# Kernel optimization log

Measured on AMD Instinct MI355X. Metric: run time of the kernel, lower is better.

## Reference

```python
import jax, jax.numpy as jnp
import numpy as np

N = 1024
NODE_DIM = 3
HIDDEN = 128
NLAYERS = 3
HEADS = 4
HD = HIDDEN // HEADS  # 32
EPS = 1e-5
NEG = -1e9


def setup_inputs() -> dict:
    key = jax.random.key(0)
    ks = jax.random.split(key, 32)
    def w(k, shape, fan_in):
        return jax.random.normal(k, shape, jnp.float32) / np.sqrt(fan_in).astype(np.float32)
    node_features = jax.random.normal(ks[0], (N, NODE_DIM), jnp.float32)
    adj = jax.random.randint(ks[1], (N, N), 0, 2).astype(jnp.float32)
    adj = adj.at[jnp.arange(N), jnp.arange(N)].set(1.0)  # self-loops
    inp = dict(
        node_features=node_features,
        adj=adj,
        Wp=w(ks[2], (NODE_DIM, HIDDEN), NODE_DIM), bp=jnp.zeros((HIDDEN,), jnp.float32),
        Wl=w(ks[3], (NLAYERS, HIDDEN, HIDDEN), HIDDEN),
        Wr=w(ks[4], (NLAYERS, HIDDEN, HIDDEN), HIDDEN),
        Wv=w(ks[5], (NLAYERS, HIDDEN, HIDDEN), HIDDEN),
        att=w(ks[6], (NLAYERS, HD), HD),
        gamma=jnp.ones((NLAYERS, HIDDEN), jnp.float32),
        beta=jnp.zeros((NLAYERS, HIDDEN), jnp.float32),
        Wn1=w(ks[7], (HIDDEN, 64), HIDDEN), bn1=jnp.zeros((64,), jnp.float32),
        Wn2=w(ks[8], (64, 1), 64), bn2=jnp.zeros((1,), jnp.float32),
        Wd1=w(ks[9], (HIDDEN, 64), HIDDEN), bd1=jnp.zeros((64,), jnp.float32),
        Wd2=w(ks[10], (64, 2), 64), bd2=jnp.zeros((2,), jnp.float32),
        Wv1=w(ks[11], (HIDDEN, 64), HIDDEN), bv1=jnp.zeros((64,), jnp.float32),
        Wv2=w(ks[12], (64, 1), 64), bv2=jnp.zeros((1,), jnp.float32),
    )
    return inp


def _gat_layer(h, mask, Wl, Wr, Wv, att, gamma, beta):
    n = h.shape[0]
    wlh = (h @ Wl).reshape(n, HEADS, HD)
    wrh = (h @ Wr).reshape(n, HEADS, HD)
    # pair[i,j,h,d] = LeakyReLU(Wl h_i + Wr h_j)  -- the O(N^2 H D) tensor
    pair = jax.nn.leaky_relu(wlh[:, None, :, :] + wrh[None, :, :, :], 0.2)
    e = jnp.einsum('ijhd,d->ijh', pair, att)
    e = jnp.where(mask[:, :, None], e, NEG)
    alpha = jax.nn.softmax(e, axis=1)  # softmax over neighbours j (dropout = identity in eval)
    v = (h @ Wv).reshape(n, HEADS, HD)
    agg = jnp.einsum('ijh,jhd->ihd', alpha, v).reshape(n, HIDDEN)
    mu = agg.mean(-1, keepdims=True)
    var = agg.var(-1, keepdims=True)
    out = (agg - mu) / jnp.sqrt(var + EPS) * gamma + beta
    return jax.nn.relu(out)


def reference(node_features, adj, Wp, bp, Wl, Wr, Wv, att, gamma, beta,
              Wn1, bn1, Wn2, bn2, Wd1, bd1, Wd2, bd2, Wv1, bv1, Wv2, bv2):
    mask = adj > 0.5
    h = jax.nn.relu(node_features @ Wp + bp)
    for l in range(NLAYERS):
        h = h + _gat_layer(h, mask, Wl[l], Wr[l], Wv[l], att[l], gamma[l], beta[l])
    node_logits = (jax.nn.relu(h @ Wn1 + bn1) @ Wn2 + bn2).squeeze(-1)
    delta_mu = jax.nn.relu(h @ Wd1 + bd1) @ Wd2 + bd2
    pooled = h.mean(axis=0)
    value = (jax.nn.relu(pooled @ Wv1 + bv1) @ Wv2 + bv2).squeeze(-1)
    return (node_logits, delta_mu, value)
```

## Files before the change

kernel.cpp:

```cpp
#include <hip/hip_runtime.h>
#include <hip/hip_bf16.h>

#define NN 1024
#define HID 128
#define NHEADS 4
#define HDD 32
#define NL 3

constexpr int OFF_CONV = 16;
constexpr int OFF_NF   = OFF_CONV;
constexpr int OFF_WP   = OFF_NF  + 3072;
constexpr int OFF_BP   = OFF_WP  + 384;
constexpr int OFF_WL   = OFF_BP  + 128;
constexpr int OFF_WR   = OFF_WL  + 49152;
constexpr int OFF_WVW  = OFF_WR  + 49152;
constexpr int OFF_ATT  = OFF_WVW + 49152;
constexpr int OFF_GAM  = OFF_ATT + 96;
constexpr int OFF_BET  = OFF_GAM + 384;
constexpr int OFF_WN1  = OFF_BET + 384;
constexpr int OFF_BN1  = OFF_WN1 + 8192;
constexpr int OFF_WN2  = OFF_BN1 + 64;
constexpr int OFF_BN2  = OFF_WN2 + 64;
constexpr int OFF_WD1  = OFF_BN2 + 1;
constexpr int OFF_BD1  = OFF_WD1 + 8192;
constexpr int OFF_WD2  = OFF_BD1 + 64;
constexpr int OFF_BD2  = OFF_WD2 + 128;
constexpr int OFF_WV1  = OFF_BD2 + 2;
constexpr int OFF_BV1  = OFF_WV1 + 8192;
constexpr int OFF_WV2  = OFF_BV1 + 64;
constexpr int OFF_BV2  = OFF_WV2 + 64;
constexpr int OFF_CONV_END = OFF_BV2 + 1;
constexpr int CONV_TOTAL = OFF_CONV_END - OFF_CONV;
constexpr int CB = (CONV_TOTAL + 255) / 256;
constexpr int OFF_MASK = 176960;
constexpr int OFF_H    = OFF_MASK + NN*32;
constexpr int OFF_WLH  = OFF_H   + NN*HID;
constexpr int OFF_WRH  = OFF_WLH + NN*HID;
constexpr int OFF_WVH  = OFF_WRH + NN*HID;
constexpr int OFF_CL   = OFF_WVH + NN*HID;
constexpr int OFF_CR   = OFF_CL  + NHEADS*NN;

__device__ __forceinline__ float bf2f(unsigned short u) {
    return __uint_as_float(((unsigned)u) << 16);
}
__device__ __forceinline__ void store_out(void* out, int idx, float v, bool bf) {
    if (bf) {
        unsigned u = __float_as_uint(v);
        unsigned r = (u + 0x7FFFu + ((u >> 16) & 1u)) >> 16;
        ((unsigned short*)out)[idx] = (unsigned short)r;
    } else {
        ((float*)out)[idx] = v;
    }
}
__device__ __forceinline__ float ldraw(const void* p, int idx, bool bf) {
    return bf ? bf2f(((const unsigned short*)p)[idx]) : ((const float*)p)[idx];
}
__device__ __forceinline__ bool detect_bf(const unsigned* nf) {
    unsigned w = nf[threadIdx.x & 63];
    int e = (int)((w >> 23) & 0xFFu);
    unsigned long long b = __ballot(e >= 110 && e <= 140);
    return __popcll(b) < 32;
}

struct P21 { const void* p[21]; };
__device__ const int g_sizes[21] = {3072,384,128,49152,49152,49152,96,384,384,
                                    8192,64,64,1,8192,64,128,2,8192,64,64,1};
__device__ const int g_dsts[21] = {OFF_NF,OFF_WP,OFF_BP,OFF_WL,OFF_WR,OFF_WVW,OFF_ATT,
                                   OFF_GAM,OFF_BET,OFF_WN1,OFF_BN1,OFF_WN2,OFF_BN2,
                                   OFF_WD1,OFF_BD1,OFF_WD2,OFF_BD2,OFF_WV1,OFF_BV1,
                                   OFF_WV2,OFF_BV2};

__global__ __launch_bounds__(256) void k_pre(P21 in, const void* adj, const unsigned* nf, float* ws) {
    bool bf = detect_bf(nf);
    int b = blockIdx.x, t = threadIdx.x;
    if (b < CB) {
        int g = b * 256 + t;
        if (g >= CONV_TOTAL) return;
        int rem = g, s = 0;
        while (s < 21 && rem >= g_sizes[s]) { rem -= g_sizes[s]; s++; }
        if (s >= 21) return;
        ws[g_dsts[s] + rem] = ldraw(in.p[s], rem, bf);
    } else if (b < CB + NN) {
        int i = b - CB;
        unsigned* mask = (unsigned*)(ws + OFF_MASK);
        int lane = t & 63, wv = t >> 6;
        #pragma unroll
        for (int q = 0; q < 4; q++) {
            int seg = wv * 4 + q;
            int j = seg * 64 + lane;
            float v = ldraw(adj, i * NN + j, bf);
            unsigned long long bl = __ballot(v > 0.5f);
            if (lane == 0) {
                mask[i * 32 + seg * 2]     = (unsigned)bl;
                mask[i * 32 + seg * 2 + 1] = (unsigned)(bl >> 32);
            }
        }
    } else {
        int bb = b - CB - NN;
        int i = bb * 2 + (t >> 7), c = t & 127;
        float a = ldraw(in.p[2], c, bf);
        #pragma unroll
        for (int k = 0; k < 3; k++)
            a += ldraw(in.p[0], i * 3 + k, bf) * ldraw(in.p[1], k * HID + c, bf);
        ws[OFF_H + i * HID + c] = fmaxf(a, 0.0f);
    }
}

__global__ __launch_bounds__(128) void k_mm3(float* ws, int l) {
    __shared__ float hs[4][HID];
    int c = threadIdx.x, i0 = blockIdx.x * 4, which = blockIdx.y;
    const float* h = ws + OFF_H;
    #pragma unroll
    for (int r = 0; r < 4; r++) hs[r][c] = h[(i0 + r) * HID + c];
    __syncthreads();
    int woff = (which == 0) ? OFF_WL : (which == 1) ? OFF_WR : OFF_WVW;
    const float* W = ws + woff + l * HID * HID;
    float a[4] = {0,0,0,0};
    #pragma unroll 4
    for (int k = 0; k < HID; k++) {
        float w = W[k * HID + c];
        #pragma unroll
        for (int r = 0; r < 4; r++) a[r] += hs[r][k] * w;
    }
    if (which == 0) {
        #pragma unroll
        for (int r = 0; r < 4; r++) ws[OFF_WLH + (i0 + r) * HID + c] = a[r];
        float att = ws[OFF_ATT + l * HDD + (c & 31)];
        #pragma unroll
        for (int r = 0; r < 4; r++) {
            float t = att * a[r];
            #pragma unroll
            for (int off = 1; off < 32; off <<= 1) t += __shfl_xor(t, off, 64);
            if ((c & 31) == 0) ws[OFF_CL + (c >> 5) * NN + (i0 + r)] = 0.6f * t;
        }
    } else {
        int doff = (which == 1) ? OFF_WRH : OFF_WVH;
        #pragma unroll
        for (int r = 0; r < 4; r++)
            ws[doff + (c >> 2) * (NN * 4) + (i0 + r) * 4 + (c & 3)] = a[r];
        if (which == 1) {
            float att = ws[OFF_ATT + l * HDD + (c & 31)];
            #pragma unroll
            for (int r = 0; r < 4; r++) {
                float t = att * a[r];
                #pragma unroll
                for (int off = 1; off < 32; off <<= 1) t += __shfl_xor(t, off, 64);
                if ((c & 31) == 0) ws[OFF_CR + (c >> 5) * NN + (i0 + r)] = 0.6f * t;
            }
        }
    }
}

__global__ __launch_bounds__(512) void k_attn(float* ws, int l) {
    int t = threadIdx.x;
    int i0 = blockIdx.x * 4;
    int lane = t & 63;
    int w = t >> 6;
    int h = __builtin_amdgcn_readfirstlane(w & 3);
    int p = __builtin_amdgcn_readfirstlane(w >> 2);
    int iA = i0 + 2 * p, iB = iA + 1;

    __shared__ unsigned mrow[4][32];
    __shared__ float ebuf[8][64][33];
    __shared__ float invs[4][4];
    __shared__ float agg_s[4][HID];
    __shared__ float red2[4][2][2];

    if (t < 128) mrow[t >> 5][t & 31] = ((const unsigned*)(ws + OFF_MASK))[i0 * 32 + t];
    __syncthreads();

    unsigned mbA = 0, mbB = 0;
    #pragma unroll
    for (int jc = 0; jc < 16; jc++) {
        int wi = jc * 2 + (lane >> 5);
        mbA |= ((mrow[2 * p][wi] >> (lane & 31)) & 1u) << jc;
        mbB |= ((mrow[2 * p + 1][wi] >> (lane & 31)) & 1u) << jc;
    }

    float att_r[32], wlA[32], wlB[32];
    const float* attp = ws + OFF_ATT + l * HDD;
    const float* wlpA = ws + OFF_WLH + iA * HID + h * HDD;
    const float* wlpB = ws + OFF_WLH + iB * HID + h * HDD;
    #pragma unroll
    for (int d = 0; d < 32; d++) {
        att_r[d] = 0.4f * attp[d];
        wlA[d] = wlpA[d];
        wlB[d] = wlpB[d];
    }
    float clA = ws[OFF_CL + h * NN + iA];
    float clB = ws[OFF_CL + h * NN + iB];

    const float* wrT = ws + OFF_WRH + h * 8 * (NN * 4) + lane * 4;
    const float* wvT = ws + OFF_WVH + h * 8 * (NN * 4) + lane * 4;
    const float* crp = ws + OFF_CR + h * NN;

    float mA = -1e30f, mB = -1e30f;
    #pragma unroll 1
    for (int jc = 0; jc < 16; jc++) {
        float cr6 = crp[jc * 64 + lane];
        float dA = 0.0f, dB = 0.0f;
        #pragma unroll
        for (int dq = 0; dq < 8; dq++) {
            float4 wv4 = *(const float4*)(wrT + dq * (NN * 4) + jc * 256);
            dA = fmaf(att_r[dq*4+0], fabsf(wlA[dq*4+0] + wv4.x), dA);
            dB = fmaf(att_r[dq*4+0], fabsf(wlB[dq*4+0] + wv4.x), dB);
            dA = fmaf(att_r[dq*4+1], fabsf(wlA[dq*4+1] + wv4.y), dA);
            dB = fmaf(att_r[dq*4+1], fabsf(wlB[dq*4+1] + wv4.y), dB);
            dA = fmaf(att_r[dq*4+2], fabsf(wlA[dq*4+2] + wv4.z), dA);
            dB = fmaf(att_r[dq*4+2], fabsf(wlB[dq*4+2] + wv4.z), dB);
            dA = fmaf(att_r[dq*4+3], fabsf(wlA[dq*4+3] + wv4.w), dA);
            dB = fmaf(att_r[dq*4+3], fabsf(wlB[dq*4+3] + wv4.w), dB);
        }
        float eA = (clA + cr6) + dA; eA = ((mbA >> jc) & 1u) ? eA : -1e9f;
        float eB = (clB + cr6) + dB; eB = ((mbB >> jc) & 1u) ? eB : -1e9f;
        ebuf[w][lane][jc]      = eA;
        ebuf[w][lane][16 + jc] = eB;
        mA = fmaxf(mA, eA);
        mB = fmaxf(mB, eB);
    }
    #pragma unroll
    for (int off = 32; off > 0; off >>= 1) {
        mA = fmaxf(mA, __shfl_xor(mA, off, 64));
        mB = fmaxf(mB, __shfl_xor(mB, off, 64));
    }

    float accA[32], accB[32];
    #pragma unroll
    for (int d = 0; d < 32; d++) { accA[d] = 0.0f; accB[d] = 0.0f; }
    float lsA = 0.0f, lsB = 0.0f;
    #pragma unroll 1
    for (int jc = 0; jc < 16; jc++) {
        float peA = __expf(ebuf[w][lane][jc]      - mA);
        float peB = __expf(ebuf[w][lane][16 + jc] - mB);
        lsA += peA; lsB += peB;
        #pragma unroll
        for (int dq = 0; dq < 8; dq++) {
            float4 v4 = *(const float4*)(wvT + dq * (NN * 4) + jc * 256);
            accA[dq*4+0] = fmaf(peA, v4.x, accA[dq*4+0]);
            accB[dq*4+0] = fmaf(peB, v4.x, accB[dq*4+0]);
            accA[dq*4+1] = fmaf(peA, v4.y, accA[dq*4+1]);
            accB[dq*4+1] = fmaf(peB, v4.y, accB[dq*4+1]);
            accA[dq*4+2] = fmaf(peA, v4.z, accA[dq*4+2]);
            accB[dq*4+2] = fmaf(peB, v4.z, accB[dq*4+2]);
            accA[dq*4+3] = fmaf(peA, v4.w, accA[dq*4+3]);
            accB[dq*4+3] = fmaf(peB, v4.w, accB[dq*4+3]);
        }
    }
    #pragma unroll
    for (int off = 32; off > 0; off >>= 1) {
        lsA += __shfl_xor(lsA, off, 64);
        lsB += __shfl_xor(lsB, off, 64);
    }
    if (lane == 0) {
        invs[2 * p][h]     = 1.0f / lsA;
        invs[2 * p + 1][h] = 1.0f / lsB;
    }
    __syncthreads();

    float* rbuf = &ebuf[0][0][0];
    {
        int reg = p * 4 + h;
        #pragma unroll
        for (int d = 0; d < 32; d++) rbuf[(reg * 64 + lane) * 33 + d] = accA[d];
        __syncthreads();
        int g = t >> 6, d = lane & 31, half = lane >> 5;
        float s = 0.0f;
        #pragma unroll
        for (int lq = 0; lq < 32; lq++) s += rbuf[(g * 64 + half * 32 + lq) * 33 + d];
        s += __shfl_xor(s, 32, 64);
        int node = 2 * (g >> 2), hh = g & 3;
        if (half == 0) agg_s[node][hh * 32 + d] = s * invs[node][hh];
        __syncthreads();
    }
    {
        int reg = p * 4 + h;
        #pragma unroll
        for (int d = 0; d < 32; d++) rbuf[(reg * 64 + lane) * 33 + d] = accB[d];
        __syncthreads();
        int g = t >> 6, d = lane & 31, half = lane >> 5;
        float s = 0.0f;
        #pragma unroll
        for (int lq = 0; lq < 32; lq++) s += rbuf[(g * 64 + half * 32 + lq) * 33 + d];
        s += __shfl_xor(s, 32, 64);
        int node = 2 * (g >> 2) + 1, hh = g & 3;
        if (half == 0) agg_s[node][hh * 32 + d] = s * invs[node][hh];
        __syncthreads();
    }

    {
        int n = t >> 7, f = t & 127;
        float agg = agg_s[n][f];
        float s = agg, s2 = agg * agg;
        #pragma unroll
        for (int off = 32; off > 0; off >>= 1) {
            s  += __shfl_xor(s,  off, 64);
            s2 += __shfl_xor(s2, off, 64);
        }
        int half = (t >> 6) & 1;
        if (lane == 0) { red2[n][half][0] = s; red2[n][half][1] = s2; }
        __syncthreads();
        float ts  = red2[n][0][0] + red2[n][1][0];
        float ts2 = red2[n][0][1] + red2[n][1][1];
        float mu  = ts  * (1.0f / HID);
        float var = ts2 * (1.0f / HID) - mu * mu;
        float gm = ws[OFF_GAM + l * HID + f];
        float be = ws[OFF_BET + l * HID + f];
        float o = (agg - mu) * rsqrtf(var + 1e-5f) * gm + be;
        ws[OFF_H + (i0 + n) * HID + f] += fmaxf(o, 0.0f);
    }
}

__global__ __launch_bounds__(1024) void k_post(float* ws, const unsigned* nf, void* out) {
    bool bf = detect_bf(nf);
    int b = blockIdx.x, t = threadIdx.x;
    if (b < 64) {
        __shared__ float hrow[16][HID];
        int n = t >> 6, tt = t & 63;
        int i = b * 16 + n;
        hrow[n][tt]      = ws[OFF_H + i * HID + tt];
        hrow[n][tt + 64] = ws[OFF_H + i * HID + tt + 64];
        __syncthreads();
        const float* Wn1 = ws + OFF_WN1;
        const float* Wd1 = ws + OFF_WD1;
        float z1 = ws[OFF_BN1 + tt], zd = ws[OFF_BD1 + tt];
        #pragma unroll 4
        for (int k = 0; k < HID; k++) {
            float hk = hrow[n][k];
            z1 += hk * Wn1[k * 64 + tt];
            zd += hk * Wd1[k * 64 + tt];
        }
        z1 = fmaxf(z1, 0.0f); zd = fmaxf(zd, 0.0f);
        float lg = z1 * ws[OFF_WN2 + tt];
        float d0 = zd * ws[OFF_WD2 + tt * 2 + 0];
        float d1 = zd * ws[OFF_WD2 + tt * 2 + 1];
        #pragma unroll
        for (int off = 32; off > 0; off >>= 1) {
            lg += __shfl_xor(lg, off, 64);
            d0 += __shfl_xor(d0, off, 64);
            d1 += __shfl_xor(d1, off, 64);
        }
        if (tt == 0) {
            store_out(out, i,              lg + ws[OFF_BN2],     bf);
            store_out(out, NN + i * 2 + 0, d0 + ws[OFF_BD2 + 0], bf);
            store_out(out, NN + i * 2 + 1, d1 + ws[OFF_BD2 + 1], bf);
        }
    } else {
        __shared__ float part[8][HID];
        __shared__ float pooled[HID];
        int g = t >> 7, c = t & 127;
        float s = 0.0f;
        #pragma unroll 16
        for (int r = 0; r < 128; r++) s += ws[OFF_H + (g * 128 + r) * HID + c];
        part[g][c] = s;
        __syncthreads();
        if (t < HID) {
            float p = 0.0f;
            #pragma unroll
            for (int gg = 0; gg < 8; gg++) p += part[gg][t];
            pooled[t] = p * (1.0f / NN);
        }
        __syncthreads();
        if (t < 64) {
            float z = ws[OFF_BV1 + t];
            float z1 = 0.0f;
            #pragma unroll 8
            for (int k = 0; k < HID; k += 2) {
                z  += pooled[k]     * ws[OFF_WV1 + k * 64 + t];
                z1 += pooled[k + 1] * ws[OFF_WV1 + (k + 1) * 64 + t];
            }
            z = fmaxf(z + z1, 0.0f);
            float pv = z * ws[OFF_WV2 + t];
            #pragma unroll
            for (int off = 32; off > 0; off >>= 1) pv += __shfl_xor(pv, off, 64);
            if (t == 0) store_out(out, 3072, pv + ws[OFF_BV2], bf);
        }
    }
}

extern "C" void kernel_launch(void* const* d_in, const int* in_sizes, int n_in,
                              void* d_out, int out_size, void* d_ws, size_t ws_size,
                              hipStream_t stream) {
    float* ws = (float*)d_ws;
    const unsigned* nf = (const unsigned*)d_in[0];

    P21 ptrs;
    const int map[21] = {0,2,3,4,5,6,7,8,9,10,11,12,13,14,15,16,17,18,19,20,21};
    for (int s = 0; s < 21; s++) ptrs.p[s] = d_in[map[s]];

    k_pre<<<CB + NN + NN / 2, 256, 0, stream>>>(ptrs, d_in[1], nf, ws);

    for (int l = 0; l < NL; l++) {
        k_mm3<<<dim3(NN / 4, 3), 128, 0, stream>>>(ws, l);
        k_attn<<<NN / 4, 512, 0, stream>>>(ws, l);
    }

    k_post<<<65, 1024, 0, stream>>>(ws, nf, d_out);
}
```

Measured before the change: 226.8 us.

## Stage Wr/Wv tiles into LDS with double-buffered async global-to-LDS loads

In the attention kernel, the per-head Wr and Wv tiles were read straight from global memory, and both wave pairs of the same head fetched the same data. Each wave now issues global_load_lds copies for half the rows of a tile into a shared, double-buffered LDS stage. The next chunk is prefetched while the current one is consumed. This halves redundant global/L2 traffic and overlaps loads with compute, at the cost of 64 KB more LDS and a block-wide barrier in every loop iteration of both passes.

```diff
diff --git a/kernel.cpp b/kernel.cpp
--- a/kernel.cpp
+++ b/kernel.cpp
@@ -61,6 +61,11 @@
     unsigned long long b = __ballot(e >= 110 && e <= 140);
     return __popcll(b) < 32;
 }
+__device__ __forceinline__ void gld_lds16(const float* g, float* l) {
+    __builtin_amdgcn_global_load_lds(
+        (const __attribute__((address_space(1))) void*)g,
+        (__attribute__((address_space(3))) void*)l, 16, 0, 0);
+}
 
 struct P21 { const void* p[21]; };
 __device__ const int g_sizes[21] = {3072,384,128,49152,49152,49152,96,384,384,
@@ -160,6 +165,7 @@
     int p = __builtin_amdgcn_readfirstlane(w >> 2);
     int iA = i0 + 2 * p, iB = iA + 1;
 
+    __shared__ float stageS[2][32][256];
     __shared__ unsigned mrow[4][32];
     __shared__ float ebuf[8][64][33];
     __shared__ float invs[4][4];
@@ -167,6 +173,29 @@
     __shared__ float red2[4][2][2];
 
     if (t < 128) mrow[t >> 5][t & 31] = ((const unsigned*)(ws + OFF_MASK))[i0 * 32 + t];
+
+    float att_r[32], wlA[32], wlB[32];
+    const float* attp = ws + OFF_ATT + l * HDD;
+    const float* wlpA = ws + OFF_WLH + iA * HID + h * HDD;
+    const float* wlpB = ws + OFF_WLH + iB * HID + h * HDD;
+    #pragma unroll
+    for (int d = 0; d < 32; d++) {
+        att_r[d] = 0.4f * attp[d];
+        wlA[d] = wlpA[d];
+        wlB[d] = wlpB[d];
+    }
+    float clA = ws[OFF_CL + h * NN + iA];
+    float clB = ws[OFF_CL + h * NN + iB];
+    const float* crp = ws + OFF_CR + h * NN;
+
+    const float* gwr = ws + OFF_WRH + (h * 8 + p * 4) * (NN * 4) + lane * 4;
+    const float* gwv = ws + OFF_WVH + (h * 8 + p * 4) * (NN * 4) + lane * 4;
+    #define STAGE(gbase, jc, buf)                                              \
+        _Pragma("unroll")                                                      \
+        for (int k = 0; k < 4; k++)                                            \
+            gld_lds16((gbase) + k * (NN * 4) + (jc) * 256,                     \
+                      &stageS[(buf)][h * 8 + p * 4 + k][0]);
+
     __syncthreads();
 
     unsigned mbA = 0, mbB = 0;
@@ -177,39 +206,27 @@
         mbB |= ((mrow[2 * p + 1][wi] >> (lane & 31)) & 1u) << jc;
     }
 
-    float att_r[32], wlA[32], wlB[32];
-    const float* attp = ws + OFF_ATT + l * HDD;
-    const float* wlpA = ws + OFF_WLH + iA * HID + h * HDD;
-    const float* wlpB = ws + OFF_WLH + iB * HID + h * HDD;
-    #pragma unroll
-    for (int d = 0; d < 32; d++) {
-        att_r[d] = 0.4f * attp[d];
-        wlA[d] = wlpA[d];
-        wlB[d] = wlpB[d];
-    }
-    float clA = ws[OFF_CL + h * NN + iA];
-    float clB = ws[OFF_CL + h * NN + iB];
-
-    const float* wrT = ws + OFF_WRH + h * 8 * (NN * 4) + lane * 4;
-    const float* wvT = ws + OFF_WVH + h * 8 * (NN * 4) + lane * 4;
-    const float* crp = ws + OFF_CR + h * NN;
-
+    STAGE(gwr, 0, 0);
+    __syncthreads();
     float mA = -1e30f, mB = -1e30f;
     #pragma unroll 1
     for (int jc = 0; jc < 16; jc++) {
+        int buf = jc & 1;
+        if (jc < 15) STAGE(gwr, jc + 1, buf ^ 1);
         float cr6 = crp[jc * 64 + lane];
+        const float4* sw = (const float4*)&stageS[buf][h * 8][0];
         float dA = 0.0f, dB = 0.0f;
         #pragma unroll
         for (int dq = 0; dq < 8; dq++) {
-            float4 wv4 = *(const float4*)(wrT + dq * (NN * 4) + jc * 256);
-            dA = fmaf(att_r[dq*4+0], fabsf(wlA[dq*4+0] + wv4.x), dA);
-            dB = fmaf(att_r[dq*4+0], fabsf(wlB[dq*4+0] + wv4.x), dB);
-            dA = fmaf(att_r[dq*4+1], fabsf(wlA[dq*4+1] + wv4.y), dA);
-            dB = fmaf(att_r[dq*4+1], fabsf(wlB[dq*4+1] + wv4.y), dB);
-            dA = fmaf(att_r[dq*4+2], fabsf(wlA[dq*4+2] + wv4.z), dA);
-            dB = fmaf(att_r[dq*4+2], fabsf(wlB[dq*4+2] + wv4.z), dB);
-            dA = fmaf(att_r[dq*4+3], fabsf(wlA[dq*4+3] + wv4.w), dA);
-            dB = fmaf(att_r[dq*4+3], fabsf(wlB[dq*4+3] + wv4.w), dB);
+            float4 w4 = sw[dq * 64 + lane];
+            dA = fmaf(att_r[dq*4+0], fabsf(wlA[dq*4+0] + w4.x), dA);
+            dB = fmaf(att_r[dq*4+0], fabsf(wlB[dq*4+0] + w4.x), dB);
+            dA = fmaf(att_r[dq*4+1], fabsf(wlA[dq*4+1] + w4.y), dA);
+            dB = fmaf(att_r[dq*4+1], fabsf(wlB[dq*4+1] + w4.y), dB);
+            dA = fmaf(att_r[dq*4+2], fabsf(wlA[dq*4+2] + w4.z), dA);
+            dB = fmaf(att_r[dq*4+2], fabsf(wlB[dq*4+2] + w4.z), dB);
+            dA = fmaf(att_r[dq*4+3], fabsf(wlA[dq*4+3] + w4.w), dA);
+            dB = fmaf(att_r[dq*4+3], fabsf(wlB[dq*4+3] + w4.w), dB);
         }
         float eA = (clA + cr6) + dA; eA = ((mbA >> jc) & 1u) ? eA : -1e9f;
         float eB = (clB + cr6) + dB; eB = ((mbB >> jc) & 1u) ? eB : -1e9f;
@@ -217,6 +234,7 @@
         ebuf[w][lane][16 + jc] = eB;
         mA = fmaxf(mA, eA);
         mB = fmaxf(mB, eB);
+        __syncthreads();
     }
     #pragma unroll
     for (int off = 32; off > 0; off >>= 1) {
@@ -224,18 +242,23 @@
         mB = fmaxf(mB, __shfl_xor(mB, off, 64));
     }
 
+    STAGE(gwv, 0, 0);
     float accA[32], accB[32];
     #pragma unroll
     for (int d = 0; d < 32; d++) { accA[d] = 0.0f; accB[d] = 0.0f; }
     float lsA = 0.0f, lsB = 0.0f;
+    __syncthreads();
     #pragma unroll 1
     for (int jc = 0; jc < 16; jc++) {
+        int buf = jc & 1;
+        if (jc < 15) STAGE(gwv, jc + 1, buf ^ 1);
         float peA = __expf(ebuf[w][lane][jc]      - mA);
         float peB = __expf(ebuf[w][lane][16 + jc] - mB);
         lsA += peA; lsB += peB;
+        const float4* sv = (const float4*)&stageS[buf][h * 8][0];
         #pragma unroll
         for (int dq = 0; dq < 8; dq++) {
-            float4 v4 = *(const float4*)(wvT + dq * (NN * 4) + jc * 256);
+            float4 v4 = sv[dq * 64 + lane];
             accA[dq*4+0] = fmaf(peA, v4.x, accA[dq*4+0]);
             accB[dq*4+0] = fmaf(peB, v4.x, accB[dq*4+0]);
             accA[dq*4+1] = fmaf(peA, v4.y, accA[dq*4+1]);
@@ -245,6 +268,7 @@
             accA[dq*4+3] = fmaf(peA, v4.w, accA[dq*4+3]);
             accB[dq*4+3] = fmaf(peB, v4.w, accB[dq*4+3]);
         }
+        __syncthreads();
     }
     #pragma unroll
     for (int off = 32; off > 0; off >>= 1) {
@@ -308,6 +332,7 @@
         float o = (agg - mu) * rsqrtf(var + 1e-5f) * gm + be;
         ws[OFF_H + (i0 + n) * HID + f] += fmaxf(o, 0.0f);
     }
+    #undef STAGE
 }
 
 __global__ __launch_bounds__(1024) void k_post(float* ws, const unsigned* nf, void* out) {
```

New measurement: 248.8 us. 9.7% more time.

## Split attention neighbour range across waves, two nodes per block

Applied to the files above, without the earlier changes.

Each k_attn block now handles 2 query nodes instead of 4. The 8 waves split the 1024 neighbours into two halves per head, rather than splitting node pairs. Partial maxima and softmax sums are combined through shared memory, and the partial accumulators are summed across the two halves. This doubles the grid to 512 blocks so the device's many CUs get more blocks, at the cost of an extra barrier and reading the Wr/Wv tiles twice as often across blocks.

```diff
diff --git a/kernel.cpp b/kernel.cpp
--- a/kernel.cpp
+++ b/kernel.cpp
@@ -153,28 +153,29 @@
 
 __global__ __launch_bounds__(512) void k_attn(float* ws, int l) {
     int t = threadIdx.x;
-    int i0 = blockIdx.x * 4;
+    int i0 = blockIdx.x * 2;
     int lane = t & 63;
     int w = t >> 6;
-    int h = __builtin_amdgcn_readfirstlane(w & 3);
-    int p = __builtin_amdgcn_readfirstlane(w >> 2);
-    int iA = i0 + 2 * p, iB = iA + 1;
-
-    __shared__ unsigned mrow[4][32];
+    int h  = __builtin_amdgcn_readfirstlane(w & 3);
+    int jh = __builtin_amdgcn_readfirstlane(w >> 2);
+    int iA = i0, iB = i0 + 1;
+
+    __shared__ unsigned mrow[2][32];
     __shared__ float ebuf[8][64][33];
-    __shared__ float invs[4][4];
-    __shared__ float agg_s[4][HID];
-    __shared__ float red2[4][2][2];
-
-    if (t < 128) mrow[t >> 5][t & 31] = ((const unsigned*)(ws + OFF_MASK))[i0 * 32 + t];
+    __shared__ float mex[2][4][2];
+    __shared__ float lsx[2][4][2];
+    __shared__ float agg_s[2][HID];
+    __shared__ float red2[2][2][2];
+
+    if (t < 64) mrow[t >> 5][t & 31] = ((const unsigned*)(ws + OFF_MASK))[i0 * 32 + t];
     __syncthreads();
 
     unsigned mbA = 0, mbB = 0;
     #pragma unroll
-    for (int jc = 0; jc < 16; jc++) {
-        int wi = jc * 2 + (lane >> 5);
-        mbA |= ((mrow[2 * p][wi] >> (lane & 31)) & 1u) << jc;
-        mbB |= ((mrow[2 * p + 1][wi] >> (lane & 31)) & 1u) << jc;
+    for (int jc = 0; jc < 8; jc++) {
+        int wi = jh * 16 + jc * 2 + (lane >> 5);
+        mbA |= ((mrow[0][wi] >> (lane & 31)) & 1u) << jc;
+        mbB |= ((mrow[1][wi] >> (lane & 31)) & 1u) << jc;
     }
 
     float att_r[32], wlA[32], wlB[32];
@@ -190,13 +191,13 @@
     float clA = ws[OFF_CL + h * NN + iA];
     float clB = ws[OFF_CL + h * NN + iB];
 
-    const float* wrT = ws + OFF_WRH + h * 8 * (NN * 4) + lane * 4;
-    const float* wvT = ws + OFF_WVH + h * 8 * (NN * 4) + lane * 4;
-    const float* crp = ws + OFF_CR + h * NN;
+    const float* wrT = ws + OFF_WRH + h * 8 * (NN * 4) + jh * 2048 + lane * 4;
+    const float* wvT = ws + OFF_WVH + h * 8 * (NN * 4) + jh * 2048 + lane * 4;
+    const float* crp = ws + OFF_CR + h * NN + jh * 512;
 
     float mA = -1e30f, mB = -1e30f;
     #pragma unroll 1
-    for (int jc = 0; jc < 16; jc++) {
+    for (int jc = 0; jc < 8; jc++) {
         float cr6 = crp[jc * 64 + lane];
         float dA = 0.0f, dB = 0.0f;
         #pragma unroll
@@ -213,8 +214,8 @@
         }
         float eA = (clA + cr6) + dA; eA = ((mbA >> jc) & 1u) ? eA : -1e9f;
         float eB = (clB + cr6) + dB; eB = ((mbB >> jc) & 1u) ? eB : -1e9f;
-        ebuf[w][lane][jc]      = eA;
-        ebuf[w][lane][16 + jc] = eB;
+        ebuf[w][lane][jc]     = eA;
+        ebuf[w][lane][8 + jc] = eB;
         mA = fmaxf(mA, eA);
         mB = fmaxf(mB, eB);
     }
@@ -223,15 +224,19 @@
         mA = fmaxf(mA, __shfl_xor(mA, off, 64));
         mB = fmaxf(mB, __shfl_xor(mB, off, 64));
     }
+    if (lane == 0) { mex[jh][h][0] = mA; mex[jh][h][1] = mB; }
+    __syncthreads();
+    mA = fmaxf(mex[0][h][0], mex[1][h][0]);
+    mB = fmaxf(mex[0][h][1], mex[1][h][1]);
 
     float accA[32], accB[32];
     #pragma unroll
     for (int d = 0; d < 32; d++) { accA[d] = 0.0f; accB[d] = 0.0f; }
     float lsA = 0.0f, lsB = 0.0f;
     #pragma unroll 1
-    for (int jc = 0; jc < 16; jc++) {
-        float peA = __expf(ebuf[w][lane][jc]      - mA);
-        float peB = __expf(ebuf[w][lane][16 + jc] - mB);
+    for (int jc = 0; jc < 8; jc++) {
+        float peA = __expf(ebuf[w][lane][jc]     - mA);
+        float peB = __expf(ebuf[w][lane][8 + jc] - mB);
         lsA += peA; lsB += peB;
         #pragma unroll
         for (int dq = 0; dq < 8; dq++) {
@@ -251,44 +256,48 @@
         lsA += __shfl_xor(lsA, off, 64);
         lsB += __shfl_xor(lsB, off, 64);
     }
-    if (lane == 0) {
-        invs[2 * p][h]     = 1.0f / lsA;
-        invs[2 * p + 1][h] = 1.0f / lsB;
-    }
-    __syncthreads();
+    if (lane == 0) { lsx[jh][h][0] = lsA; lsx[jh][h][1] = lsB; }
 
     float* rbuf = &ebuf[0][0][0];
     {
-        int reg = p * 4 + h;
-        #pragma unroll
-        for (int d = 0; d < 32; d++) rbuf[(reg * 64 + lane) * 33 + d] = accA[d];
-        __syncthreads();
-        int g = t >> 6, d = lane & 31, half = lane >> 5;
-        float s = 0.0f;
-        #pragma unroll
-        for (int lq = 0; lq < 32; lq++) s += rbuf[(g * 64 + half * 32 + lq) * 33 + d];
-        s += __shfl_xor(s, 32, 64);
-        int node = 2 * (g >> 2), hh = g & 3;
-        if (half == 0) agg_s[node][hh * 32 + d] = s * invs[node][hh];
+        #pragma unroll
+        for (int d = 0; d < 32; d++) rbuf[(w * 64 + lane) * 33 + d] = accA[d];
+        __syncthreads();
+        int g = t >> 6, d = lane & 31, halfl = lane >> 5;
+        if (g < 4) {
+            float s = 0.0f;
+            #pragma unroll
+            for (int lq = 0; lq < 32; lq++) {
+                s += rbuf[(g * 64       + halfl * 32 + lq) * 33 + d];
+                s += rbuf[((g + 4) * 64 + halfl * 32 + lq) * 33 + d];
+            }
+            s += __shfl_xor(s, 32, 64);
+            if (halfl == 0)
+                agg_s[0][g * 32 + d] = s * (1.0f / (lsx[0][g][0] + lsx[1][g][0]));
+        }
         __syncthreads();
     }
     {
-        int reg = p * 4 + h;
-        #pragma unroll
-        for (int d = 0; d < 32; d++) rbuf[(reg * 64 + lane) * 33 + d] = accB[d];
-        __syncthreads();
-        int g = t >> 6, d = lane & 31, half = lane >> 5;
-        float s = 0.0f;
-        #pragma unroll
-        for (int lq = 0; lq < 32; lq++) s += rbuf[(g * 64 + half * 32 + lq) * 33 + d];
-        s += __shfl_xor(s, 32, 64);
-        int node = 2 * (g >> 2) + 1, hh = g & 3;
-        if (half == 0) agg_s[node][hh * 32 + d] = s * invs[node][hh];
+        #pragma unroll
+        for (int d = 0; d < 32; d++) rbuf[(w * 64 + lane) * 33 + d] = accB[d];
+        __syncthreads();
+        int g = t >> 6, d = lane & 31, halfl = lane >> 5;
+        if (g < 4) {
+            float s = 0.0f;
+            #pragma unroll
+            for (int lq = 0; lq < 32; lq++) {
+                s += rbuf[(g * 64       + halfl * 32 + lq) * 33 + d];
+                s += rbuf[((g + 4) * 64 + halfl * 32 + lq) * 33 + d];
+            }
+            s += __shfl_xor(s, 32, 64);
+            if (halfl == 0)
+                agg_s[1][g * 32 + d] = s * (1.0f / (lsx[0][g][1] + lsx[1][g][1]));
+        }
         __syncthreads();
     }
 
     {
-        int n = t >> 7, f = t & 127;
+        int n = (t >> 7) & 1, f = t & 127;
         float agg = agg_s[n][f];
         float s = agg, s2 = agg * agg;
         #pragma unroll
@@ -296,8 +305,8 @@
             s  += __shfl_xor(s,  off, 64);
             s2 += __shfl_xor(s2, off, 64);
         }
-        int half = (t >> 6) & 1;
-        if (lane == 0) { red2[n][half][0] = s; red2[n][half][1] = s2; }
+        int halfw = (t >> 6) & 1;
+        if (lane == 0 && t < 256) { red2[n][halfw][0] = s; red2[n][halfw][1] = s2; }
         __syncthreads();
         float ts  = red2[n][0][0] + red2[n][1][0];
         float ts2 = red2[n][0][1] + red2[n][1][1];
@@ -306,7 +315,7 @@
         float gm = ws[OFF_GAM + l * HID + f];
         float be = ws[OFF_BET + l * HID + f];
         float o = (agg - mu) * rsqrtf(var + 1e-5f) * gm + be;
-        ws[OFF_H + (i0 + n) * HID + f] += fmaxf(o, 0.0f);
+        if (t < 256) ws[OFF_H + (i0 + n) * HID + f] += fmaxf(o, 0.0f);
     }
 }
 
@@ -391,7 +400,7 @@
 
     for (int l = 0; l < NL; l++) {
         k_mm3<<<dim3(NN / 4, 3), 128, 0, stream>>>(ws, l);
-        k_attn<<<NN / 4, 512, 0, stream>>>(ws, l);
+        k_attn<<<NN / 2, 512, 0, stream>>>(ws, l);
     }
 
     k_post<<<65, 1024, 0, stream>>>(ws, nf, d_out);
```

Result: no change. 227.2 us (+0.2%).

## Split head dims across wave pairs so each wave handles four nodes

Applied to the files above, without the earlier changes.

The attention kernel now splits each head's 32 dims into two 16-dim halves, one per wave, and each wave processes all four query nodes instead of two. Partial attention logits go to shared memory and are summed with the partner wave's half before the softmax. This halves the Wr/Wv loads per wave for each node processed and doubles the reuse of each loaded float4. The cost is a larger shared buffer, an extra barrier, and more shared-memory reads during the softmax passes.

```diff
diff --git a/kernel.cpp b/kernel.cpp
--- a/kernel.cpp
+++ b/kernel.cpp
@@ -156,12 +156,11 @@
     int i0 = blockIdx.x * 4;
     int lane = t & 63;
     int w = t >> 6;
-    int h = __builtin_amdgcn_readfirstlane(w & 3);
-    int p = __builtin_amdgcn_readfirstlane(w >> 2);
-    int iA = i0 + 2 * p, iB = iA + 1;
-
+    int h  = __builtin_amdgcn_readfirstlane(w & 3);
+    int dh = __builtin_amdgcn_readfirstlane(w >> 2);
+
+    __shared__ float pbuf[8][64][66];
     __shared__ unsigned mrow[4][32];
-    __shared__ float ebuf[8][64][33];
     __shared__ float invs[4][4];
     __shared__ float agg_s[4][HID];
     __shared__ float red2[4][2][2];
@@ -169,123 +168,127 @@
     if (t < 128) mrow[t >> 5][t & 31] = ((const unsigned*)(ws + OFF_MASK))[i0 * 32 + t];
     __syncthreads();
 
-    unsigned mbA = 0, mbB = 0;
-    #pragma unroll
-    for (int jc = 0; jc < 16; jc++) {
-        int wi = jc * 2 + (lane >> 5);
-        mbA |= ((mrow[2 * p][wi] >> (lane & 31)) & 1u) << jc;
-        mbB |= ((mrow[2 * p + 1][wi] >> (lane & 31)) & 1u) << jc;
-    }
-
-    float att_r[32], wlA[32], wlB[32];
-    const float* attp = ws + OFF_ATT + l * HDD;
-    const float* wlpA = ws + OFF_WLH + iA * HID + h * HDD;
-    const float* wlpB = ws + OFF_WLH + iB * HID + h * HDD;
-    #pragma unroll
-    for (int d = 0; d < 32; d++) {
-        att_r[d] = 0.4f * attp[d];
-        wlA[d] = wlpA[d];
-        wlB[d] = wlpB[d];
-    }
-    float clA = ws[OFF_CL + h * NN + iA];
-    float clB = ws[OFF_CL + h * NN + iB];
-
-    const float* wrT = ws + OFF_WRH + h * 8 * (NN * 4) + lane * 4;
-    const float* wvT = ws + OFF_WVH + h * 8 * (NN * 4) + lane * 4;
+    unsigned mb[4];
+    #pragma unroll
+    for (int n = 0; n < 4; n++) {
+        unsigned m = 0;
+        #pragma unroll
+        for (int jc = 0; jc < 16; jc++)
+            m |= ((mrow[n][jc * 2 + (lane >> 5)] >> (lane & 31)) & 1u) << jc;
+        mb[n] = m;
+    }
+
+    float att_r[16], wl[4][16], cl[4];
+    const float* attp = ws + OFF_ATT + l * HDD + dh * 16;
+    #pragma unroll
+    for (int d = 0; d < 16; d++) att_r[d] = 0.4f * attp[d];
+    #pragma unroll
+    for (int n = 0; n < 4; n++) {
+        const float* wlp = ws + OFF_WLH + (i0 + n) * HID + h * HDD + dh * 16;
+        #pragma unroll
+        for (int d = 0; d < 16; d++) wl[n][d] = wlp[d];
+        cl[n] = ws[OFF_CL + h * NN + i0 + n];
+    }
+
+    const float* wrT = ws + OFF_WRH + (h * 8 + dh * 4) * (NN * 4) + lane * 4;
+    const float* wvT = ws + OFF_WVH + (h * 8 + dh * 4) * (NN * 4) + lane * 4;
     const float* crp = ws + OFF_CR + h * NN;
 
-    float mA = -1e30f, mB = -1e30f;
     #pragma unroll 1
     for (int jc = 0; jc < 16; jc++) {
         float cr6 = crp[jc * 64 + lane];
-        float dA = 0.0f, dB = 0.0f;
-        #pragma unroll
-        for (int dq = 0; dq < 8; dq++) {
-            float4 wv4 = *(const float4*)(wrT + dq * (NN * 4) + jc * 256);
-            dA = fmaf(att_r[dq*4+0], fabsf(wlA[dq*4+0] + wv4.x), dA);
-            dB = fmaf(att_r[dq*4+0], fabsf(wlB[dq*4+0] + wv4.x), dB);
-            dA = fmaf(att_r[dq*4+1], fabsf(wlA[dq*4+1] + wv4.y), dA);
-            dB = fmaf(att_r[dq*4+1], fabsf(wlB[dq*4+1] + wv4.y), dB);
-            dA = fmaf(att_r[dq*4+2], fabsf(wlA[dq*4+2] + wv4.z), dA);
-            dB = fmaf(att_r[dq*4+2], fabsf(wlB[dq*4+2] + wv4.z), dB);
-            dA = fmaf(att_r[dq*4+3], fabsf(wlA[dq*4+3] + wv4.w), dA);
-            dB = fmaf(att_r[dq*4+3], fabsf(wlB[dq*4+3] + wv4.w), dB);
-        }
-        float eA = (clA + cr6) + dA; eA = ((mbA >> jc) & 1u) ? eA : -1e9f;
-        float eB = (clB + cr6) + dB; eB = ((mbB >> jc) & 1u) ? eB : -1e9f;
-        ebuf[w][lane][jc]      = eA;
-        ebuf[w][lane][16 + jc] = eB;
-        mA = fmaxf(mA, eA);
-        mB = fmaxf(mB, eB);
-    }
-    #pragma unroll
-    for (int off = 32; off > 0; off >>= 1) {
-        mA = fmaxf(mA, __shfl_xor(mA, off, 64));
-        mB = fmaxf(mB, __shfl_xor(mB, off, 64));
-    }
-
-    float accA[32], accB[32];
-    #pragma unroll
-    for (int d = 0; d < 32; d++) { accA[d] = 0.0f; accB[d] = 0.0f; }
-    float lsA = 0.0f, lsB = 0.0f;
+        float dot[4] = {0.f, 0.f, 0.f, 0.f};
+        #pragma unroll
+        for (int k = 0; k < 4; k++) {
+            float4 w4 = *(const float4*)(wrT + k * (NN * 4) + jc * 256);
+            #pragma unroll
+            for (int n = 0; n < 4; n++) {
+                dot[n] = fmaf(att_r[k*4+0], fabsf(wl[n][k*4+0] + w4.x), dot[n]);
+                dot[n] = fmaf(att_r[k*4+1], fabsf(wl[n][k*4+1] + w4.y), dot[n]);
+                dot[n] = fmaf(att_r[k*4+2], fabsf(wl[n][k*4+2] + w4.z), dot[n]);
+                dot[n] = fmaf(att_r[k*4+3], fabsf(wl[n][k*4+3] + w4.w), dot[n]);
+            }
+        }
+        #pragma unroll
+        for (int n = 0; n < 4; n++) {
+            float pv = dot[n];
+            if (dh == 0) pv += cl[n] + cr6;
+            pbuf[w][lane][jc * 4 + n] = pv;
+        }
+    }
+    __syncthreads();
+
+    int wp = w ^ 4;
+    float m4[4] = {-1e30f, -1e30f, -1e30f, -1e30f};
     #pragma unroll 1
     for (int jc = 0; jc < 16; jc++) {
-        float peA = __expf(ebuf[w][lane][jc]      - mA);
-        float peB = __expf(ebuf[w][lane][16 + jc] - mB);
-        lsA += peA; lsB += peB;
-        #pragma unroll
-        for (int dq = 0; dq < 8; dq++) {
-            float4 v4 = *(const float4*)(wvT + dq * (NN * 4) + jc * 256);
-            accA[dq*4+0] = fmaf(peA, v4.x, accA[dq*4+0]);
-            accB[dq*4+0] = fmaf(peB, v4.x, accB[dq*4+0]);
-            accA[dq*4+1] = fmaf(peA, v4.y, accA[dq*4+1]);
-            accB[dq*4+1] = fmaf(peB, v4.y, accB[dq*4+1]);
-            accA[dq*4+2] = fmaf(peA, v4.z, accA[dq*4+2]);
-            accB[dq*4+2] = fmaf(peB, v4.z, accB[dq*4+2]);
-            accA[dq*4+3] = fmaf(peA, v4.w, accA[dq*4+3]);
-            accB[dq*4+3] = fmaf(peB, v4.w, accB[dq*4+3]);
+        #pragma unroll
+        for (int n = 0; n < 4; n++) {
+            float e = pbuf[w][lane][jc * 4 + n] + pbuf[wp][lane][jc * 4 + n];
+            e = ((mb[n] >> jc) & 1u) ? e : -1e9f;
+            m4[n] = fmaxf(m4[n], e);
         }
     }
     #pragma unroll
     for (int off = 32; off > 0; off >>= 1) {
-        lsA += __shfl_xor(lsA, off, 64);
-        lsB += __shfl_xor(lsB, off, 64);
-    }
-    if (lane == 0) {
-        invs[2 * p][h]     = 1.0f / lsA;
-        invs[2 * p + 1][h] = 1.0f / lsB;
-    }
-    __syncthreads();
-
-    float* rbuf = &ebuf[0][0][0];
+        #pragma unroll
+        for (int n = 0; n < 4; n++) m4[n] = fmaxf(m4[n], __shfl_xor(m4[n], off, 64));
+    }
+
+    float acc[4][16];
+    #pragma unroll
+    for (int n = 0; n < 4; n++)
+        #pragma unroll
+        for (int d = 0; d < 16; d++) acc[n][d] = 0.0f;
+    float ls[4] = {0.f, 0.f, 0.f, 0.f};
+    #pragma unroll 1
+    for (int jc = 0; jc < 16; jc++) {
+        float pe[4];
+        #pragma unroll
+        for (int n = 0; n < 4; n++) {
+            float e = pbuf[w][lane][jc * 4 + n] + pbuf[wp][lane][jc * 4 + n];
+            e = ((mb[n] >> jc) & 1u) ? e : -1e9f;
+            pe[n] = __expf(e - m4[n]);
+            ls[n] += pe[n];
+        }
+        #pragma unroll
+        for (int k = 0; k < 4; k++) {
+            float4 v4 = *(const float4*)(wvT + k * (NN * 4) + jc * 256);
+            #pragma unroll
+            for (int n = 0; n < 4; n++) {
+                acc[n][k*4+0] = fmaf(pe[n], v4.x, acc[n][k*4+0]);
+                acc[n][k*4+1] = fmaf(pe[n], v4.y, acc[n][k*4+1]);
+                acc[n][k*4+2] = fmaf(pe[n], v4.z, acc[n][k*4+2]);
+                acc[n][k*4+3] = fmaf(pe[n], v4.w, acc[n][k*4+3]);
+            }
+        }
+    }
+    #pragma unroll
+    for (int off = 32; off > 0; off >>= 1) {
+        #pragma unroll
+        for (int n = 0; n < 4; n++) ls[n] += __shfl_xor(ls[n], off, 64);
+    }
+    if (dh == 0 && lane == 0) {
+        #pragma unroll
+        for (int n = 0; n < 4; n++) invs[n][h] = 1.0f / ls[n];
+    }
+    __syncthreads();
+
+    #pragma unroll
+    for (int n = 0; n < 4; n++)
+        #pragma unroll
+        for (int d = 0; d < 16; d++) pbuf[w][lane][n * 16 + d] = acc[n][d];
+    __syncthreads();
     {
-        int reg = p * 4 + h;
-        #pragma unroll
-        for (int d = 0; d < 32; d++) rbuf[(reg * 64 + lane) * 33 + d] = accA[d];
-        __syncthreads();
-        int g = t >> 6, d = lane & 31, half = lane >> 5;
-        float s = 0.0f;
-        #pragma unroll
-        for (int lq = 0; lq < 32; lq++) s += rbuf[(g * 64 + half * 32 + lq) * 33 + d];
-        s += __shfl_xor(s, 32, 64);
-        int node = 2 * (g >> 2), hh = g & 3;
-        if (half == 0) agg_s[node][hh * 32 + d] = s * invs[node][hh];
-        __syncthreads();
-    }
-    {
-        int reg = p * 4 + h;
-        #pragma unroll
-        for (int d = 0; d < 32; d++) rbuf[(reg * 64 + lane) * 33 + d] = accB[d];
-        __syncthreads();
-        int g = t >> 6, d = lane & 31, half = lane >> 5;
-        float s = 0.0f;
-        #pragma unroll
-        for (int lq = 0; lq < 32; lq++) s += rbuf[(g * 64 + half * 32 + lq) * 33 + d];
-        s += __shfl_xor(s, 32, 64);
-        int node = 2 * (g >> 2) + 1, hh = g & 3;
-        if (half == 0) agg_s[node][hh * 32 + d] = s * invs[node][hh];
-        __syncthreads();
-    }
+        int g = t >> 6, s = lane;
+        float sum = 0.0f;
+        #pragma unroll 8
+        for (int lq = 0; lq < 64; lq++) sum += pbuf[g][lq][s];
+        int gh = g & 3, gdh = g >> 2;
+        int n = s >> 4, dd = s & 15;
+        agg_s[n][gh * 32 + gdh * 16 + dd] = sum * invs[n][gh];
+    }
+    __syncthreads();
 
     {
         int n = t >> 7, f = t & 127;
```

Measured after the change: 239.8 us. 5.7% more time.
